# Kernel tuning notes

Hardware: AMD Instinct MI355X
Metric: run time of the kernel (lower is better)

Reference implementation:

```python
import jax, jax.numpy as jnp
import numpy as np

TAU = 0.01          # init_temperature
N_CODEWORDS = 512
EPS = 1e-10


def setup_inputs() -> dict:
    key = jax.random.key(0)
    k1, k2, k3 = jax.random.split(key, 3)
    B, C, H, W = 8, 256, 64, 64
    K = N_CODEWORDS
    feats = jax.random.normal(k1, (B, C, H, W), dtype=jnp.float32)
    codebook = jax.random.normal(k2, (K, C), dtype=jnp.float32)
    # standard Gumbel(0,1) noise, matching torch's F.gumbel_softmax sampling
    gumbel_noise = jax.random.gumbel(k3, (B, H * W, K), dtype=jnp.float32)
    return {"feats": feats, "codebook": codebook, "gumbel_noise": gumbel_noise}


def reference(feats, codebook, gumbel_noise):
    B, C, H, W = feats.shape
    K = codebook.shape[0]
    N = H * W
    # (B, C, H, W) -> (B, N, C) tokens
    f = feats.reshape(B, C, N).transpose(0, 2, 1)
    # affinity[b,n,k] = ((f[b,n,:] - cb[k,:]).sum(-1))**2
    # sum over channels commutes with the subtraction, so reduce first
    # instead of materializing the (B, N, K, C) broadcast the torch code builds.
    sf = f.sum(axis=-1)            # (B, N)
    sw = codebook.sum(axis=-1)     # (K,)
    affinity = (sf[:, :, None] - sw[None, None, :]) ** 2   # (B, N, K)
    logits = jnp.exp(-affinity)
    # gumbel-softmax (soft, hard=False), tau = TAU, over codeword axis
    soft_one_hot = jax.nn.softmax((logits + gumbel_noise) / TAU, axis=2)
    qy = jax.nn.softmax(logits, axis=2)
    kld_loss = jnp.sum(qy * jnp.log(qy * K + EPS), axis=2).mean()
    codewords = jnp.argmax(soft_one_hot, axis=2).reshape(B, H, W)
    # weighted codeword sum: (B, N, K) @ (K, C) -> (B, N, C)
    sel = jnp.einsum("bnk,kc->bnc", soft_one_hot, codebook)
    sel_codewords = sel.transpose(0, 2, 1).reshape(B, C, H, W)
    mat_id_probs = soft_one_hot.transpose(0, 2, 1).reshape(B, K, H, W)
    return (sel_codewords, codewords, kld_loss, mat_id_probs)
```

## Files before the change

kernel.cpp:

```cpp
#include <hip/hip_runtime.h>
#include <math.h>
#include <stdint.h>

#define NB  8
#define NC  256
#define NHW 4096
#define NK  512

#define OFF_SEL 0ULL
#define OFF_CW  8388608ULL
#define OFF_KLD 8421376ULL
#define OFF_MAT 8421377ULL
#define MAT_COUNT 16777216ULL
#define OUT_TOTAL (OFF_MAT + MAT_COUNT)

typedef float f4v __attribute__((ext_vector_type(4)));


__global__ void gumbel_prep(const float* __restrict__ cb, double* __restrict__ ws) {
    const int l = threadIdx.x & 63;
    const int w = threadIdx.x >> 6;
    const int k = blockIdx.x * 4 + w;
    const float4 v = *reinterpret_cast<const float4*>(cb + (size_t)k * NC + l * 4);
    double s = (double)v.x + (double)v.y + (double)v.z + (double)v.w;
    #pragma unroll
    for (int off = 32; off > 0; off >>= 1) s += __shfl_xor(s, off);
    if (l == 0) ws[k] = s;
    if (blockIdx.x == 0 && threadIdx.x == 0) ws[NK] = 0.0;
}

__global__ void zmat(float* __restrict__ out) {
    const size_t base4 = 2105345ULL;
    const size_t n4    = 4194303ULL;
    size_t i = (size_t)blockIdx.x * blockDim.x + threadIdx.x;
    const size_t stride = (size_t)gridDim.x * blockDim.x;
    f4v* o4 = reinterpret_cast<f4v*>(out) + base4;
    const f4v z = {0.f, 0.f, 0.f, 0.f};
    for (; i < n4; i += stride) __builtin_nontemporal_store(z, o4 + i);
    if (blockIdx.x == 0 && threadIdx.x < 4) {
        out[OFF_MAT + threadIdx.x] = 0.f;
        if (threadIdx.x == 0) out[OUT_TOTAL - 1] = 0.f;
    }
}

__global__ void __launch_bounds__(512, 4)
gs_main(const float* __restrict__ feats, const float* __restrict__ gumbel,
        const float* __restrict__ cb, double* __restrict__ ws,
        float* __restrict__ out) {
    __shared__ double part[8][64];
    __shared__ float  sw_f[NK];
    __shared__ double sf_d[64];
    __shared__ float  sf_f[64];
    __shared__ int    kcnt[64];
    __shared__ int    klist[64][17];
    __shared__ float  wlist[64][17];
    __shared__ double kldp[8];

    const int tid = threadIdx.x;
    const int l   = tid & 63;
    const int w   = tid >> 6;
    const int b   = blockIdx.x >> 6;
    const int n0  = (blockIdx.x & 63) * 64;

    {
        const float* fp = feats + ((size_t)b * NC + w * 32) * NHW + n0 + l;
        double s = 0.0;
        #pragma unroll
        for (int i = 0; i < 32; ++i) s += (double)fp[(size_t)i * NHW];
        part[w][l] = s;
        sw_f[tid] = (float)ws[tid];
        __syncthreads();
        if (tid < 64) {
            double a = 0.0;
            #pragma unroll
            for (int i = 0; i < 8; ++i) a += part[i][tid];
            sf_d[tid] = a; sf_f[tid] = (float)a;
            kcnt[tid] = 0;
        }
        __syncthreads();
    }

    float swreg[8];
    #pragma unroll
    for (int jj = 0; jj < 8; ++jj) swreg[jj] = sw_f[l + 64 * jj];

    double kld_wave = 0.0;
    float gc[8], gn[8];
    {
        const float* gp = gumbel + ((size_t)(b * NHW) + n0 + w * 8) * NK;
        #pragma unroll
        for (int jj = 0; jj < 8; ++jj) gc[jj] = gp[l + 64 * jj];
    }
    #pragma unroll
    for (int i = 0; i < 8; ++i) {
        const int tt = w * 8 + i;
        const int n  = n0 + tt;
        if (i < 7) {
            const float* gpn = gumbel + ((size_t)(b * NHW) + n + 1) * NK;
            #pragma unroll
            for (int jj = 0; jj < 8; ++jj) gn[jj] = gpn[l + 64 * jj];
        }
        const float sft = sf_f[tt];
        float y[8];
        float M = -1.0e30f, YS = -1.0e30f; int KB = 0;
        float E = 0.f, T = 0.f;
        #pragma unroll
        for (int jj = 0; jj < 8; ++jj) {
            const int k = l + 64 * jj;
            const float d = sft - swreg[jj];
            const float logit = __expf(-d * d);
            const float yy = logit + gc[jj];
            y[jj] = yy;
            const float h = fmaf(logit, fmaf(logit, fmaf(logit, fmaf(logit,
                              1.f/120.f, 1.f/24.f), 1.f/6.f), 0.5f), 1.f);
            const float xh = logit * h;
            E += xh;
            T = fmaf(logit, 1.f + xh, T);
            if (yy > M) { YS = M; M = yy; KB = k; }
            else YS = fmaxf(YS, yy);
        }
        #pragma unroll
        for (int off = 32; off > 0; off >>= 1) {
            const float oM = __shfl_xor(M, off);
            const int   oK = __shfl_xor(KB, off);
            const float oY = __shfl_xor(YS, off);
            const float oE = __shfl_xor(E, off);
            const float oT = __shfl_xor(T, off);
            const float nys = fmaxf(fmaxf(YS, oY), fminf(M, oM));
            if (oM > M || (oM == M && oK < KB)) { M = oM; KB = oK; }
            YS = nys; E += oE; T += oT;
        }
        E += 512.f;

        if (M - YS < 5e-3f) {
            const double sfd = sf_d[tt];
            double ym64 = -1.0e300; int kb64 = 0;
            #pragma unroll
            for (int jj = 0; jj < 8; ++jj) {
                const int k = l + 64 * jj;
                const double dd = sfd - ws[k];
                const double aff = dd * dd;
                const double lg = (aff < 45.0) ? exp(-aff) : 0.0;
                const double yy = lg + (double)gc[jj];
                if (yy > ym64) { ym64 = yy; kb64 = k; }
            }
            #pragma unroll
            for (int off = 32; off > 0; off >>= 1) {
                const double oy = __shfl_xor(ym64, off);
                const int    ok = __shfl_xor(kb64, off);
                if (oy > ym64 || (oy == ym64 && ok < kb64)) { ym64 = oy; kb64 = ok; }
            }
            KB = kb64;
        }
        if (l == 0) {
            out[OFF_CW + (size_t)b * NHW + n] = (float)KB;
            kld_wave += (double)(T / E + 6.2383246250395075f - logf(E));
        }

        float pr[8]; float Sl = 0.f;
        #pragma unroll
        for (int jj = 0; jj < 8; ++jj) {
            const float p = __expf((y[jj] - M) * 100.0f);
            pr[jj] = p; Sl += p;
        }
        #pragma unroll
        for (int off = 32; off > 0; off >>= 1) Sl += __shfl_xor(Sl, off);
        const float inv = 1.0f / Sl;

        #pragma unroll
        for (int jj = 0; jj < 8; ++jj) {
            if (pr[jj] > 4e-8f) {
                const int k = l + 64 * jj;
                const float wgt = pr[jj] * inv;
                out[OFF_MAT + ((size_t)b * NK + k) * NHW + n] = wgt;
                const int idx = atomicAdd(&kcnt[tt], 1);
                if (idx < 16) { klist[tt][idx] = k; wlist[tt][idx] = wgt; }
            }
        }
        #pragma unroll
        for (int jj = 0; jj < 8; ++jj) gc[jj] = gn[jj];
    }
    if (l == 0) kldp[w] = kld_wave;
    __syncthreads();
    if (tid == 0) {
        double acc = 0.0;
        #pragma unroll
        for (int i = 0; i < 8; ++i) acc += kldp[i];
        atomicAdd(&ws[NK], acc);
    }

    {
        const int cnt = min(kcnt[l], 16);
        #pragma unroll
        for (int half = 0; half < 2; ++half) {
            float acc[16];
            #pragma unroll
            for (int i2 = 0; i2 < 16; ++i2) acc[i2] = 0.f;
            for (int e = 0; e < cnt; ++e) {
                const int k = klist[l][e];
                const float wgt = wlist[l][e];
                const float4* cr = reinterpret_cast<const float4*>(
                    cb + (size_t)k * NC + w * 32 + half * 16);
                #pragma unroll
                for (int q = 0; q < 4; ++q) {
                    const float4 v = cr[q];
                    acc[q * 4 + 0] += wgt * v.x; acc[q * 4 + 1] += wgt * v.y;
                    acc[q * 4 + 2] += wgt * v.z; acc[q * 4 + 3] += wgt * v.w;
                }
            }
            float* basep = out + OFF_SEL + ((size_t)b * NC + w * 32 + half * 16) * NHW + n0 + l;
            #pragma unroll
            for (int i2 = 0; i2 < 16; ++i2)
                __builtin_nontemporal_store(acc[i2], basep + (size_t)i2 * NHW);
        }
    }
}

__global__ void gumbel_fin(const double* __restrict__ ws, float* __restrict__ out) {
    out[OFF_KLD] = (float)(ws[NK] * (1.0 / 32768.0));
}

extern "C" void kernel_launch(void* const* d_in, const int* in_sizes, int n_in,
                              void* d_out, int out_size, void* d_ws, size_t ws_size,
                              hipStream_t stream) {
    const float* feats = (const float*)d_in[0];
    const float* cb    = (const float*)d_in[1];
    const float* gum   = (const float*)d_in[2];
    double* ws = (double*)d_ws;
    float* out = (float*)d_out;
    gumbel_prep<<<128, 256, 0, stream>>>(cb, ws);
    zmat<<<2048, 256, 0, stream>>>(out);
    gs_main<<<512, 512, 0, stream>>>(feats, gum, cb, ws, out);
    gumbel_fin<<<1, 1, 0, stream>>>(ws, out);
}
```

Measured before the change: 67.36 us.

## Process two tokens per wave with half-wave DPP reductions and deferred softmax normalization

```diff
diff --git a/kernel.cpp b/kernel.cpp
--- a/kernel.cpp
+++ b/kernel.cpp
@@ -16,6 +16,21 @@
 
 typedef float f4v __attribute__((ext_vector_type(4)));
 
+
+template <int C>
+__device__ __forceinline__ float fdpp(float x) {
+    return __int_as_float(__builtin_amdgcn_update_dpp(0, __float_as_int(x), C, 0xF, 0xF, true));
+}
+template <int C>
+__device__ __forceinline__ int idpp(int x) {
+    return __builtin_amdgcn_update_dpp(0, x, C, 0xF, 0xF, true);
+}
+__device__ __forceinline__ float fswz16(float x) {
+    return __int_as_float(__builtin_amdgcn_ds_swizzle(__float_as_int(x), 0x401F));
+}
+__device__ __forceinline__ int iswz16(int x) {
+    return __builtin_amdgcn_ds_swizzle(x, 0x401F);
+}
 
 __global__ void gumbel_prep(const float* __restrict__ cb, double* __restrict__ ws) {
     const int l = threadIdx.x & 63;
@@ -52,8 +67,8 @@
     __shared__ double sf_d[64];
     __shared__ float  sf_f[64];
     __shared__ int    kcnt[64];
-    __shared__ int    klist[64][17];
-    __shared__ float  wlist[64][17];
+    __shared__ int    klist[64][25];
+    __shared__ float  wlist[64][25];
     __shared__ double kldp[8];
 
     const int tid = threadIdx.x;
@@ -80,33 +95,35 @@
         __syncthreads();
     }
 
-    float swreg[8];
+    const int lh = l & 31;
+    const int hb = l >> 5;
+    float swreg[16];
     #pragma unroll
-    for (int jj = 0; jj < 8; ++jj) swreg[jj] = sw_f[l + 64 * jj];
-
-    double kld_wave = 0.0;
-    float gc[8], gn[8];
-    {
-        const float* gp = gumbel + ((size_t)(b * NHW) + n0 + w * 8) * NK;
-        #pragma unroll
-        for (int jj = 0; jj < 8; ++jj) gc[jj] = gp[l + 64 * jj];
+    for (int jj = 0; jj < 16; ++jj) swreg[jj] = sw_f[lh + 32 * jj];
+
+    double kld_loc = 0.0;
+    float gc[16], gn[16];
+    {
+        const float* gp = gumbel + ((size_t)(b * NHW) + n0 + w * 8 + hb) * NK;
+        #pragma unroll
+        for (int jj = 0; jj < 16; ++jj) gc[jj] = gp[lh + 32 * jj];
     }
     #pragma unroll
-    for (int i = 0; i < 8; ++i) {
-        const int tt = w * 8 + i;
+    for (int i = 0; i < 4; ++i) {
+        const int tt = w * 8 + 2 * i + hb;
         const int n  = n0 + tt;
-        if (i < 7) {
-            const float* gpn = gumbel + ((size_t)(b * NHW) + n + 1) * NK;
-            #pragma unroll
-            for (int jj = 0; jj < 8; ++jj) gn[jj] = gpn[l + 64 * jj];
+        if (i < 3) {
+            const float* gpn = gumbel + ((size_t)(b * NHW) + n + 2) * NK;
+            #pragma unroll
+            for (int jj = 0; jj < 16; ++jj) gn[jj] = gpn[lh + 32 * jj];
         }
         const float sft = sf_f[tt];
-        float y[8];
+        float y[16];
         float M = -1.0e30f, YS = -1.0e30f; int KB = 0;
         float E = 0.f, T = 0.f;
         #pragma unroll
-        for (int jj = 0; jj < 8; ++jj) {
-            const int k = l + 64 * jj;
+        for (int jj = 0; jj < 16; ++jj) {
+            const int k = lh + 32 * jj;
             const float d = sft - swreg[jj];
             const float logit = __expf(-d * d);
             const float yy = logit + gc[jj];
@@ -119,25 +136,26 @@
             if (yy > M) { YS = M; M = yy; KB = k; }
             else YS = fmaxf(YS, yy);
         }
-        #pragma unroll
-        for (int off = 32; off > 0; off >>= 1) {
-            const float oM = __shfl_xor(M, off);
-            const int   oK = __shfl_xor(KB, off);
-            const float oY = __shfl_xor(YS, off);
-            const float oE = __shfl_xor(E, off);
-            const float oT = __shfl_xor(T, off);
-            const float nys = fmaxf(fmaxf(YS, oY), fminf(M, oM));
-            if (oM > M || (oM == M && oK < KB)) { M = oM; KB = oK; }
-            YS = nys; E += oE; T += oT;
-        }
+        #define BSTEP(GF, GI) { \
+            const float oM = GF(M); const int oK = GI(KB); \
+            const float oY = GF(YS); const float oE = GF(E); const float oT = GF(T); \
+            const float nys = fmaxf(fmaxf(YS, oY), fminf(M, oM)); \
+            if (oM > M || (oM == M && oK < KB)) { M = oM; KB = oK; } \
+            YS = nys; E += oE; T += oT; }
+        BSTEP(fdpp<0xB1>,  idpp<0xB1>)
+        BSTEP(fdpp<0x4E>,  idpp<0x4E>)
+        BSTEP(fdpp<0x141>, idpp<0x141>)
+        BSTEP(fdpp<0x140>, idpp<0x140>)
+        BSTEP(fswz16,      iswz16)
+        #undef BSTEP
         E += 512.f;
 
         if (M - YS < 5e-3f) {
             const double sfd = sf_d[tt];
             double ym64 = -1.0e300; int kb64 = 0;
             #pragma unroll
-            for (int jj = 0; jj < 8; ++jj) {
-                const int k = l + 64 * jj;
+            for (int jj = 0; jj < 16; ++jj) {
+                const int k = lh + 32 * jj;
                 const double dd = sfd - ws[k];
                 const double aff = dd * dd;
                 const double lg = (aff < 45.0) ? exp(-aff) : 0.0;
@@ -145,42 +163,34 @@
                 if (yy > ym64) { ym64 = yy; kb64 = k; }
             }
             #pragma unroll
-            for (int off = 32; off > 0; off >>= 1) {
+            for (int off = 1; off < 32; off <<= 1) {
                 const double oy = __shfl_xor(ym64, off);
                 const int    ok = __shfl_xor(kb64, off);
                 if (oy > ym64 || (oy == ym64 && ok < kb64)) { ym64 = oy; kb64 = ok; }
             }
             KB = kb64;
         }
-        if (l == 0) {
+        if (lh == 0) {
             out[OFF_CW + (size_t)b * NHW + n] = (float)KB;
-            kld_wave += (double)(T / E + 6.2383246250395075f - logf(E));
-        }
-
-        float pr[8]; float Sl = 0.f;
-        #pragma unroll
-        for (int jj = 0; jj < 8; ++jj) {
+            kld_loc += (double)(T / E + 6.2383246250395075f - logf(E));
+        }
+
+        #pragma unroll
+        for (int jj = 0; jj < 16; ++jj) {
             const float p = __expf((y[jj] - M) * 100.0f);
-            pr[jj] = p; Sl += p;
-        }
-        #pragma unroll
-        for (int off = 32; off > 0; off >>= 1) Sl += __shfl_xor(Sl, off);
-        const float inv = 1.0f / Sl;
-
-        #pragma unroll
-        for (int jj = 0; jj < 8; ++jj) {
-            if (pr[jj] > 4e-8f) {
-                const int k = l + 64 * jj;
-                const float wgt = pr[jj] * inv;
-                out[OFF_MAT + ((size_t)b * NK + k) * NHW + n] = wgt;
+            if (p > 4e-8f) {
                 const int idx = atomicAdd(&kcnt[tt], 1);
-                if (idx < 16) { klist[tt][idx] = k; wlist[tt][idx] = wgt; }
-            }
-        }
-        #pragma unroll
-        for (int jj = 0; jj < 8; ++jj) gc[jj] = gn[jj];
-    }
-    if (l == 0) kldp[w] = kld_wave;
+                if (idx < 24) { klist[tt][idx] = lh + 32 * jj; wlist[tt][idx] = p; }
+            }
+        }
+        #pragma unroll
+        for (int jj = 0; jj < 16; ++jj) gc[jj] = gn[jj];
+    }
+    {
+        double kd = kld_loc;
+        kd += __shfl_xor(kd, 32);
+        if (l == 0) kldp[w] = kd;
+    }
     __syncthreads();
     if (tid == 0) {
         double acc = 0.0;
@@ -189,8 +199,23 @@
         atomicAdd(&ws[NK], acc);
     }
 
-    {
-        const int cnt = min(kcnt[l], 16);
+    if (tid < 64) {
+        const int cnt = min(kcnt[tid], 24);
+        float S = 0.f;
+        for (int e = 0; e < cnt; ++e) S += wlist[tid][e];
+        const float inv = 1.f / S;
+        float* orow = out + OFF_MAT + ((size_t)b * NK) * NHW + n0 + tid;
+        for (int e = 0; e < cnt; ++e) {
+            const float wgt = wlist[tid][e] * inv;
+            wlist[tid][e] = wgt;
+            orow[(size_t)klist[tid][e] * NHW] = wgt;
+        }
+        kcnt[tid] = cnt;
+    }
+    __syncthreads();
+
+    {
+        const int cnt = kcnt[l];
         #pragma unroll
         for (int half = 0; half < 2; ++half) {
             float acc[16];
```

New measurement: 77.71 us. 15.4% more time.
